# Kernel optimization log

Hardware: AMD Instinct MI355X
Metric: run time of the kernel (lower is better)

The kernel has to match this reference:

```python
import jax, jax.numpy as jnp
import numpy as np
from jax import lax

FILTER_SIZE = 11
N_ITER = 5


def gaussian_kernel1d(inv_theta, spacing, size):
    # distances = spacing * [-(size//2) .. size//2]; zero out center tap
    d = spacing * jnp.arange(-(size // 2), size // 2 + 1, dtype=jnp.float32)
    k = jnp.exp(-(d * inv_theta) ** 2 / 2)
    return k.at[size // 2].set(0.0)


def conv_along_axis(x, kernel, axis):
    # x: (C, *spatial); 1D conv along `axis`, 'same' padding (kernel symmetric -> corr == conv)
    x = jnp.moveaxis(x, axis, -1)
    shp = x.shape
    x2 = x.reshape(-1, 1, shp[-1])  # (M, 1, L)
    K = kernel.shape[0]
    out = lax.conv_general_dilated(
        x2, kernel[None, None, :].astype(x2.dtype), (1,), [(K // 2, K // 2)],
        dimension_numbers=('NCH', 'OIH', 'NCH'))
    return jnp.moveaxis(out.reshape(shp), -1, axis)


def _gaussian_filter_single(xi, inv_theta, spacing):
    # xi: (C, H, W); separable gaussian with per-sample spacing
    for i in range(2):
        k = gaussian_kernel1d(inv_theta[i], spacing[i], FILTER_SIZE)
        xi = conv_along_axis(xi, k, i + 1)
    return xi


_smooth = jax.vmap(_gaussian_filter_single, in_axes=(0, None, 0))


def reference(x, spatial_spacings, smoothness_weight, inv_smoothness_theta):
    n_classes = x.shape[1]
    comp = -jnp.eye(n_classes, dtype=x.dtype)  # -(label_i == label_j)
    negative_unary = x
    for _ in range(N_ITER):
        p = jax.nn.softmax(x, axis=1)
        s = smoothness_weight * _smooth(p, inv_smoothness_theta, spatial_spacings)
        c = jnp.einsum('bchw,cd->bdhw', s, comp)
        x = negative_unary - c
    return jax.nn.log_softmax(x, axis=1)


def setup_inputs() -> dict:
    key = jax.random.key(0)
    k1, = jax.random.split(key, 1)
    B, C, H, W = 16, 16, 384, 384
    return {
        'x': jax.random.normal(k1, (B, C, H, W), dtype=jnp.float32),
        'spatial_spacings': jnp.ones((B, 2), dtype=jnp.float32),
        'smoothness_weight': jnp.asarray(1.0, dtype=jnp.float32),
        'inv_smoothness_theta': jnp.ones((2,), dtype=jnp.float32),
    }
```

## Files before the change

### kernel.cpp

```cpp
#include <hip/hip_runtime.h>

#define BB 16
#define CC 16
#define HH 384
#define WW 384
#define HWSZ (HH*WW)
#define CHW (CC*HWSZ)
#define NPIX (BB*CHW)
#define KS 11

#define K2_THREADS 256
#define K2_HSEGS 24
#define K2_SEGH (HH/K2_HSEGS)
#define W8 (WW/8)
#define ROWU4 (WW/8)

typedef unsigned short ushortT;

__device__ __forceinline__ float bf2f(ushortT h) {
    union { unsigned u; float f; } c; c.u = ((unsigned)h) << 16; return c.f;
}
__device__ __forceinline__ ushortT f2bf(float f) {
    union { float f; unsigned u; } c; c.f = f;
    unsigned r = c.u + 0x7FFFu + ((c.u >> 16) & 1u);
    return (ushortT)(r >> 16);
}
__device__ __forceinline__ void unpk2(unsigned u, float& lo, float& hi) {
    union { unsigned u; float f; } a, b;
    a.u = u << 16; b.u = u & 0xFFFF0000u;
    lo = a.f; hi = b.f;
}
__device__ __forceinline__ unsigned pk2(float lo, float hi) {
    return ((unsigned)f2bf(hi) << 16) | (unsigned)f2bf(lo);
}

__global__ __launch_bounds__(256) void k_cvt(const float* __restrict__ x0,
                                             ushortT* __restrict__ x0b)
{
    const int i = blockIdx.x * 256 + threadIdx.x;
    if (i >= NPIX / 8) return;
    const float4 a = ((const float4*)x0)[2 * i];
    const float4 b = ((const float4*)x0)[2 * i + 1];
    uint4 o;
    o.x = pk2(a.x, a.y); o.y = pk2(a.z, a.w);
    o.z = pk2(b.x, b.y); o.w = pk2(b.z, b.w);
    ((uint4*)x0b)[i] = o;
}

__global__ __launch_bounds__(WW) void k_smax_convw(
    const ushortT* __restrict__ xin, ushortT* __restrict__ t,
    const float* __restrict__ spacings, const float* __restrict__ invtheta)
{
    const int h = blockIdx.x;
    const int b = blockIdx.y;
    const int w = threadIdx.x;
    __shared__ float p[CC][WW];

    const ushortT* xb = xin + (size_t)b * CHW + (size_t)h * WW + w;
    float v[CC];
#pragma unroll
    for (int c = 0; c < CC; ++c) v[c] = bf2f(xb[(size_t)c * HWSZ]);

    float m = v[0];
#pragma unroll
    for (int c = 1; c < CC; ++c) m = fmaxf(m, v[c]);
    float s = 0.f;
#pragma unroll
    for (int c = 0; c < CC; ++c) { v[c] = __expf(v[c] - m); s += v[c]; }
    const float inv = 1.0f / s;
#pragma unroll
    for (int c = 0; c < CC; ++c) p[c][w] = v[c] * inv;

    const float sc = spacings[b * 2 + 1] * invtheta[1];
    float kw[KS];
#pragma unroll
    for (int j = 0; j < KS; ++j) { float d = sc * (float)(j - 5); kw[j] = __expf(-0.5f * d * d); }
    kw[5] = 0.f;

    __syncthreads();

    ushortT* tb = t + (size_t)b * CHW + (size_t)h * WW + w;
#pragma unroll
    for (int c = 0; c < CC; ++c) {
        float acc = 0.f;
#pragma unroll
        for (int j = 0; j < KS; ++j) {
            if (j == 5) continue;
            const int ww = w + j - 5;
            const float pv = (ww >= 0 && ww < WW) ? p[c][ww] : 0.f;
            acc = fmaf(kw[j], pv, acc);
        }
        tb[(size_t)c * HWSZ] = f2bf(acc);
    }
}

__global__ __launch_bounds__(K2_THREADS) void k_convh_add(
    const ushortT* __restrict__ t, const ushortT* __restrict__ x0b,
    ushortT* __restrict__ xout,
    const float* __restrict__ spacings, const float* __restrict__ invtheta,
    const float* __restrict__ swp)
{
    const int colIdx = blockIdx.x * K2_THREADS + threadIdx.x;
    const int c  = colIdx / W8;
    const int w8 = colIdx - c * W8;
    const int b  = blockIdx.z;
    const int h0 = blockIdx.y * K2_SEGH;

    const float sw = swp[0];
    const float sc = spacings[b * 2 + 0] * invtheta[0];
    float kh[KS];
#pragma unroll
    for (int j = 0; j < KS; ++j) { float d = sc * (float)(j - 5); kh[j] = __expf(-0.5f * d * d); }
    kh[5] = 0.f;

    const size_t base = (size_t)(b * CC + c) * HWSZ + (size_t)w8 * 8;
    const uint4* tb = (const uint4*)(t    + base);
    const uint4* ub = (const uint4*)(x0b  + base);
    uint4*       ob = (uint4*)      (xout + base);

    const uint4 z4 = make_uint4(0u, 0u, 0u, 0u);
    uint4 win[KS];
#pragma unroll
    for (int j = 0; j < KS; ++j) {
        const int r = h0 + j - 5;
        win[j] = ((unsigned)r < HH) ? tb[(size_t)r * ROWU4] : z4;
    }

#pragma unroll 4
    for (int h = h0; h < h0 + K2_SEGH; ++h) {
        const int nr = h + 6;
        const uint4 nt = (nr < HH) ? tb[(size_t)nr * ROWU4] : z4;
        const uint4 u  = ub[(size_t)h * ROWU4];

        float acc[8];
#pragma unroll
        for (int k = 0; k < 8; ++k) acc[k] = 0.f;
#pragma unroll
        for (int j = 0; j < KS; ++j) {
            if (j == 5) continue;
            float e0, e1, e2, e3, e4, e5, e6, e7;
            unpk2(win[j].x, e0, e1); unpk2(win[j].y, e2, e3);
            unpk2(win[j].z, e4, e5); unpk2(win[j].w, e6, e7);
            const float kj = kh[j];
            acc[0] = fmaf(kj, e0, acc[0]); acc[1] = fmaf(kj, e1, acc[1]);
            acc[2] = fmaf(kj, e2, acc[2]); acc[3] = fmaf(kj, e3, acc[3]);
            acc[4] = fmaf(kj, e4, acc[4]); acc[5] = fmaf(kj, e5, acc[5]);
            acc[6] = fmaf(kj, e6, acc[6]); acc[7] = fmaf(kj, e7, acc[7]);
        }
        float u0, u1, u2, u3, u4, u5, u6, u7;
        unpk2(u.x, u0, u1); unpk2(u.y, u2, u3);
        unpk2(u.z, u4, u5); unpk2(u.w, u6, u7);
        uint4 o;
        o.x = pk2(fmaf(sw, acc[0], u0), fmaf(sw, acc[1], u1));
        o.y = pk2(fmaf(sw, acc[2], u2), fmaf(sw, acc[3], u3));
        o.z = pk2(fmaf(sw, acc[4], u4), fmaf(sw, acc[5], u5));
        o.w = pk2(fmaf(sw, acc[6], u6), fmaf(sw, acc[7], u7));
        ob[(size_t)h * ROWU4] = o;

#pragma unroll
        for (int j = 0; j < KS - 1; ++j) win[j] = win[j + 1];
        win[KS - 1] = nt;
    }
}

__global__ __launch_bounds__(256) void k_final(
    const ushortT* __restrict__ xf, float* __restrict__ out)
{
    const int p4 = blockIdx.x * 256 + threadIdx.x;
    if (p4 >= (BB * HWSZ) / 4) return;
    const int b  = p4 / (HWSZ / 4);
    const int r4 = p4 - b * (HWSZ / 4);
    const size_t base = (size_t)b * CHW + (size_t)r4 * 4;

    float v[CC][4];
#pragma unroll
    for (int c = 0; c < CC; ++c) {
        const uint2 u = *(const uint2*)(xf + base + (size_t)c * HWSZ);
        unpk2(u.x, v[c][0], v[c][1]);
        unpk2(u.y, v[c][2], v[c][3]);
    }
#pragma unroll
    for (int k = 0; k < 4; ++k) {
        float m = v[0][k];
#pragma unroll
        for (int c = 1; c < CC; ++c) m = fmaxf(m, v[c][k]);
        float s = 0.f;
#pragma unroll
        for (int c = 0; c < CC; ++c) s += __expf(v[c][k] - m);
        const float l = m + __logf(s);
#pragma unroll
        for (int c = 0; c < CC; ++c) v[c][k] -= l;
    }
#pragma unroll
    for (int c = 0; c < CC; ++c) {
        float4 o = make_float4(v[c][0], v[c][1], v[c][2], v[c][3]);
        *(float4*)(out + base + (size_t)c * HWSZ) = o;
    }
}

extern "C" void kernel_launch(void* const* d_in, const int* in_sizes, int n_in,
                              void* d_out, int out_size, void* d_ws, size_t ws_size,
                              hipStream_t stream)
{
    const float* x0   = (const float*)d_in[0];
    const float* spac = (const float*)d_in[1];
    const float* sw   = (const float*)d_in[2];
    const float* it   = (const float*)d_in[3];

    ushortT* x0b = (ushortT*)d_ws;
    ushortT* t   = x0b + (size_t)NPIX;
    ushortT* xb  = (ushortT*)d_out;
    float*   out = (float*)d_out;

    k_cvt<<<(NPIX / 8 + 255) / 256, 256, 0, stream>>>(x0, x0b);

    dim3 g1(HH, BB);
    dim3 g2(CC * W8 / K2_THREADS, K2_HSEGS, BB);

    for (int n = 0; n < 5; ++n) {
        k_smax_convw<<<g1, dim3(WW), 0, stream>>>(n == 0 ? x0b : xb, t, spac, it);
        k_convh_add<<<g2, dim3(K2_THREADS), 0, stream>>>(
            t, x0b, (n == 4) ? x0b : xb, spac, it, sw);
    }
    const int np4 = (BB * HWSZ) / 4;
    k_final<<<(np4 + 255) / 256, 256, 0, stream>>>(x0b, out);
}
```

Measured before the change: 486.1 us.

## Vectorize softmax+W-conv via wave shuffles, fuse fp32->bf16 conversion, halve H segments

Rewrites the softmax/width-convolution kernel so each thread handles 8 contiguous pixels via 16-byte loads, and exchanges neighbour halos with wavefront shuffles instead of staging probabilities in shared memory. The first iteration reads fp32 input directly and writes the bf16 copy, removing the separate conversion kernel and its extra pass. The H-conv kernel also uses half as many height segments. Risks: 16 of 64 lanes idle in each wave, and softmax exponentials are rounded to bf16 before normalization, which adds precision loss.

```diff
diff --git a/kernel.cpp b/kernel.cpp
--- a/kernel.cpp
+++ b/kernel.cpp
@@ -10,7 +10,7 @@
 #define KS 11
 
 #define K2_THREADS 256
-#define K2_HSEGS 24
+#define K2_HSEGS 12
 #define K2_SEGH (HH/K2_HSEGS)
 #define W8 (WW/8)
 #define ROWU4 (WW/8)
@@ -33,43 +33,29 @@
 __device__ __forceinline__ unsigned pk2(float lo, float hi) {
     return ((unsigned)f2bf(hi) << 16) | (unsigned)f2bf(lo);
 }
-
-__global__ __launch_bounds__(256) void k_cvt(const float* __restrict__ x0,
-                                             ushortT* __restrict__ x0b)
-{
-    const int i = blockIdx.x * 256 + threadIdx.x;
-    if (i >= NPIX / 8) return;
-    const float4 a = ((const float4*)x0)[2 * i];
-    const float4 b = ((const float4*)x0)[2 * i + 1];
-    uint4 o;
-    o.x = pk2(a.x, a.y); o.y = pk2(a.z, a.w);
-    o.z = pk2(b.x, b.y); o.w = pk2(b.z, b.w);
-    ((uint4*)x0b)[i] = o;
-}
-
-__global__ __launch_bounds__(WW) void k_smax_convw(
-    const ushortT* __restrict__ xin, ushortT* __restrict__ t,
+__device__ __forceinline__ void unpk8(const uint4& q, float* v) {
+    unpk2(q.x, v[0], v[1]); unpk2(q.y, v[2], v[3]);
+    unpk2(q.z, v[4], v[5]); unpk2(q.w, v[6], v[7]);
+}
+__device__ __forceinline__ uint4 pk8(const float* v) {
+    uint4 q;
+    q.x = pk2(v[0], v[1]); q.y = pk2(v[2], v[3]);
+    q.z = pk2(v[4], v[5]); q.w = pk2(v[6], v[7]);
+    return q;
+}
+
+template<bool F32IN>
+__global__ __launch_bounds__(256) void k_smax_convw_v(
+    const void* __restrict__ xin, ushortT* __restrict__ t,
+    ushortT* __restrict__ x0b,
     const float* __restrict__ spacings, const float* __restrict__ invtheta)
 {
-    const int h = blockIdx.x;
-    const int b = blockIdx.y;
-    const int w = threadIdx.x;
-    __shared__ float p[CC][WW];
-
-    const ushortT* xb = xin + (size_t)b * CHW + (size_t)h * WW + w;
-    float v[CC];
-#pragma unroll
-    for (int c = 0; c < CC; ++c) v[c] = bf2f(xb[(size_t)c * HWSZ]);
-
-    float m = v[0];
-#pragma unroll
-    for (int c = 1; c < CC; ++c) m = fmaxf(m, v[c]);
-    float s = 0.f;
-#pragma unroll
-    for (int c = 0; c < CC; ++c) { v[c] = __expf(v[c] - m); s += v[c]; }
-    const float inv = 1.0f / s;
-#pragma unroll
-    for (int c = 0; c < CC; ++c) p[c][w] = v[c] * inv;
+    const int lane = threadIdx.x & 63;
+    const int r    = threadIdx.x >> 6;
+    const int h    = blockIdx.x * 4 + r;
+    const int b    = blockIdx.y;
+    const bool act = lane < 48;
+    const int g    = act ? lane : 0;
 
     const float sc = spacings[b * 2 + 1] * invtheta[1];
     float kw[KS];
@@ -77,20 +63,82 @@
     for (int j = 0; j < KS; ++j) { float d = sc * (float)(j - 5); kw[j] = __expf(-0.5f * d * d); }
     kw[5] = 0.f;
 
-    __syncthreads();
-
-    ushortT* tb = t + (size_t)b * CHW + (size_t)h * WW + w;
-#pragma unroll
-    for (int c = 0; c < CC; ++c) {
-        float acc = 0.f;
-#pragma unroll
-        for (int j = 0; j < KS; ++j) {
-            if (j == 5) continue;
-            const int ww = w + j - 5;
-            const float pv = (ww >= 0 && ww < WW) ? p[c][ww] : 0.f;
-            acc = fmaf(kw[j], pv, acc);
+    const size_t base = (size_t)b * CHW + (size_t)h * WW + (size_t)g * 8;
+
+    uint4 xq[CC];
+    if (F32IN) {
+        const float* xf = (const float*)xin;
+#pragma unroll
+        for (int c = 0; c < CC; ++c) {
+            const float4 A = *(const float4*)(xf + base + (size_t)c * HWSZ);
+            const float4 B = *(const float4*)(xf + base + (size_t)c * HWSZ + 4);
+            uint4 q;
+            q.x = pk2(A.x, A.y); q.y = pk2(A.z, A.w);
+            q.z = pk2(B.x, B.y); q.w = pk2(B.z, B.w);
+            xq[c] = q;
+            if (act) *(uint4*)(x0b + base + (size_t)c * HWSZ) = q;
         }
-        tb[(size_t)c * HWSZ] = f2bf(acc);
+    } else {
+        const ushortT* xb = (const ushortT*)xin;
+#pragma unroll
+        for (int c = 0; c < CC; ++c)
+            xq[c] = *(const uint4*)(xb + base + (size_t)c * HWSZ);
+    }
+
+    float m[8];
+    unpk8(xq[0], m);
+#pragma unroll
+    for (int c = 1; c < CC; ++c) {
+        float v[8]; unpk8(xq[c], v);
+#pragma unroll
+        for (int k = 0; k < 8; ++k) m[k] = fmaxf(m[k], v[k]);
+    }
+
+    float s[8];
+#pragma unroll
+    for (int k = 0; k < 8; ++k) s[k] = 0.f;
+#pragma unroll
+    for (int c = 0; c < CC; ++c) {
+        float v[8]; unpk8(xq[c], v);
+#pragma unroll
+        for (int k = 0; k < 8; ++k) { v[k] = __expf(v[k] - m[k]); s[k] += v[k]; }
+        xq[c] = pk8(v);
+    }
+    float inv[8];
+#pragma unroll
+    for (int k = 0; k < 8; ++k) inv[k] = 1.0f / s[k];
+
+    ushortT* tb = t + base;
+#pragma unroll
+    for (int c = 0; c < CC; ++c) {
+        float p[8]; unpk8(xq[c], p);
+#pragma unroll
+        for (int k = 0; k < 8; ++k) p[k] *= inv[k];
+
+        float win[18];
+        win[0] = __shfl_up(p[3], 1); win[1] = __shfl_up(p[4], 1);
+        win[2] = __shfl_up(p[5], 1); win[3] = __shfl_up(p[6], 1);
+        win[4] = __shfl_up(p[7], 1);
+        win[13] = __shfl_down(p[0], 1); win[14] = __shfl_down(p[1], 1);
+        win[15] = __shfl_down(p[2], 1); win[16] = __shfl_down(p[3], 1);
+        win[17] = __shfl_down(p[4], 1);
+        if (g == 0)  { win[0] = win[1] = win[2] = win[3] = win[4] = 0.f; }
+        if (g == 47) { win[13] = win[14] = win[15] = win[16] = win[17] = 0.f; }
+#pragma unroll
+        for (int k = 0; k < 8; ++k) win[5 + k] = p[k];
+
+        float o[8];
+#pragma unroll
+        for (int k = 0; k < 8; ++k) {
+            float acc = 0.f;
+#pragma unroll
+            for (int j = 0; j < KS; ++j) {
+                if (j == 5) continue;
+                acc = fmaf(kw[j], win[k + j], acc);
+            }
+            o[k] = acc;
+        }
+        if (act) *(uint4*)(tb + (size_t)c * HWSZ) = pk8(o);
     }
 }
 
@@ -122,8 +170,8 @@
     uint4 win[KS];
 #pragma unroll
     for (int j = 0; j < KS; ++j) {
-        const int r = h0 + j - 5;
-        win[j] = ((unsigned)r < HH) ? tb[(size_t)r * ROWU4] : z4;
+        const int rr = h0 + j - 5;
+        win[j] = ((unsigned)rr < HH) ? tb[(size_t)rr * ROWU4] : z4;
     }
 
 #pragma unroll 4
@@ -138,24 +186,16 @@
 #pragma unroll
         for (int j = 0; j < KS; ++j) {
             if (j == 5) continue;
-            float e0, e1, e2, e3, e4, e5, e6, e7;
-            unpk2(win[j].x, e0, e1); unpk2(win[j].y, e2, e3);
-            unpk2(win[j].z, e4, e5); unpk2(win[j].w, e6, e7);
+            float e[8]; unpk8(win[j], e);
             const float kj = kh[j];
-            acc[0] = fmaf(kj, e0, acc[0]); acc[1] = fmaf(kj, e1, acc[1]);
-            acc[2] = fmaf(kj, e2, acc[2]); acc[3] = fmaf(kj, e3, acc[3]);
-            acc[4] = fmaf(kj, e4, acc[4]); acc[5] = fmaf(kj, e5, acc[5]);
-            acc[6] = fmaf(kj, e6, acc[6]); acc[7] = fmaf(kj, e7, acc[7]);
+#pragma unroll
+            for (int k = 0; k < 8; ++k) acc[k] = fmaf(kj, e[k], acc[k]);
         }
-        float u0, u1, u2, u3, u4, u5, u6, u7;
-        unpk2(u.x, u0, u1); unpk2(u.y, u2, u3);
-        unpk2(u.z, u4, u5); unpk2(u.w, u6, u7);
-        uint4 o;
-        o.x = pk2(fmaf(sw, acc[0], u0), fmaf(sw, acc[1], u1));
-        o.y = pk2(fmaf(sw, acc[2], u2), fmaf(sw, acc[3], u3));
-        o.z = pk2(fmaf(sw, acc[4], u4), fmaf(sw, acc[5], u5));
-        o.w = pk2(fmaf(sw, acc[6], u6), fmaf(sw, acc[7], u7));
-        ob[(size_t)h * ROWU4] = o;
+        float uu[8]; unpk8(u, uu);
+        float o[8];
+#pragma unroll
+        for (int k = 0; k < 8; ++k) o[k] = fmaf(sw, acc[k], uu[k]);
+        ob[(size_t)h * ROWU4] = pk8(o);
 
 #pragma unroll
         for (int j = 0; j < KS - 1; ++j) win[j] = win[j + 1];
@@ -212,13 +252,14 @@
     ushortT* xb  = (ushortT*)d_out;
     float*   out = (float*)d_out;
 
-    k_cvt<<<(NPIX / 8 + 255) / 256, 256, 0, stream>>>(x0, x0b);
-
-    dim3 g1(HH, BB);
+    dim3 g1(HH / 4, BB);
     dim3 g2(CC * W8 / K2_THREADS, K2_HSEGS, BB);
 
-    for (int n = 0; n < 5; ++n) {
-        k_smax_convw<<<g1, dim3(WW), 0, stream>>>(n == 0 ? x0b : xb, t, spac, it);
+    k_smax_convw_v<true><<<g1, dim3(256), 0, stream>>>(x0, t, x0b, spac, it);
+    k_convh_add<<<g2, dim3(K2_THREADS), 0, stream>>>(t, x0b, xb, spac, it, sw);
+
+    for (int n = 1; n < 5; ++n) {
+        k_smax_convw_v<false><<<g1, dim3(256), 0, stream>>>(xb, t, x0b, spac, it);
         k_convh_add<<<g2, dim3(K2_THREADS), 0, stream>>>(
             t, x0b, (n == 4) ? x0b : xb, spac, it, sw);
     }
```

Measured after the change: 524.0 us. +7.8%, slower.
